# Optimization experiments

Measured on AMD Instinct MI355X. Metric: run time of the kernel, lower is better.

## Reference

```python
import jax, jax.numpy as jnp
import numpy as np
import math

B, L, HID = 2, 2048, 1024
NH, DH = 16, 64
MASK_VAL = -1000000000.0  # half_precision_flag == False


def setup_inputs() -> dict:
    key = jax.random.key(0)
    ks = jax.random.split(key, 12)
    s = 0.02
    return {
        "queries": jax.random.normal(ks[0], (B, L, HID), jnp.float32),
        "keys": jax.random.normal(ks[1], (B, L, HID), jnp.float32),
        "values": jax.random.normal(ks[2], (B, L, HID), jnp.float32),
        "mask": jax.random.randint(ks[3], (B, L, L), 0, 2, jnp.int32),
        "Wq": jax.random.normal(ks[4], (HID, NH * DH), jnp.float32) * s,
        "bq": jnp.zeros((NH * DH,), jnp.float32),
        "Wk": jax.random.normal(ks[5], (HID, NH * DH), jnp.float32) * s,
        "bk": jnp.zeros((NH * DH,), jnp.float32),
        "Wv": jax.random.normal(ks[6], (HID, NH * DH), jnp.float32) * s,
        "bv": jnp.zeros((NH * DH,), jnp.float32),
        "Wo": jax.random.normal(ks[7], (NH * DH, HID), jnp.float32) * s,
        "bo": jnp.zeros((HID,), jnp.float32),
    }


def reference(queries, keys, values, mask, Wq, bq, Wk, bk, Wv, bv, Wo, bo):
    # Linear projections: (B, L, NH*DH)
    q = queries @ Wq + bq
    k = keys @ Wk + bk
    v = values @ Wv + bv
    # FAITHFUL to original: raw .view(B, NH, -1, DH) without transpose
    q = q.reshape(B, NH, L, DH)
    k = k.reshape(B, NH, L, DH)
    v = v.reshape(B, NH, L, DH)
    # scaled dot-product scores: (B, NH, L, L)
    scores = jnp.einsum("bhqd,bhkd->bhqk", q, k) / math.sqrt(DH)
    scores = jnp.where(mask[:, None, :, :] == 0, MASK_VAL, scores)
    probs = jax.nn.softmax(scores, axis=-1)  # dropout p=0 -> identity
    ctx = jnp.einsum("bhqk,bhkd->bhqd", probs, v)  # (B, NH, L, DH)
    # transpose(1,2) then flatten heads, as in original
    ctx = ctx.transpose(0, 2, 1, 3).reshape(B, L, NH * DH)
    return ctx @ Wo + bo
```

## Files before the change

kernel.cpp:

```cpp
#include <hip/hip_runtime.h>
#include <stdint.h>

typedef __bf16 bf16;
typedef __bf16 bf16x8 __attribute__((ext_vector_type(8)));
typedef __bf16 bf16x4 __attribute__((ext_vector_type(4)));
typedef float  f32x4  __attribute__((ext_vector_type(4)));
typedef short  s16x4  __attribute__((ext_vector_type(4)));
typedef unsigned long long ull;

#define GLOAD16(gptr, lptr)                                                     \
  __builtin_amdgcn_global_load_lds(                                             \
      (const __attribute__((address_space(1))) void*)(gptr),                    \
      (__attribute__((address_space(3))) void*)(lptr), 16, 0, 0)

#define MFMA16(a, b, c) __builtin_amdgcn_mfma_f32_16x16x32_bf16((a), (b), (c), 0, 0, 0)
#define MFMA16K16(a, b, c) __builtin_amdgcn_mfma_f32_16x16x16bf16_1k((a), (b), (c), 0, 0, 0)

static constexpr int B_ = 2, L_ = 2048, NH_ = 16, DH_ = 64;
static constexpr float QSCALE = 0.18033688011112042f;

__global__ __launch_bounds__(256) void k_prep(const float* __restrict__ q,
                                              const float* __restrict__ k,
                                              const float* __restrict__ v,
                                              const int* __restrict__ mask,
                                              const float* __restrict__ wq,
                                              const float* __restrict__ wk,
                                              const float* __restrict__ wv,
                                              const float* __restrict__ wo,
                                              bf16* __restrict__ X,
                                              bf16* __restrict__ Wt,
                                              ull* __restrict__ mb) {
  __shared__ float t[32][33];
  const int bid = blockIdx.x, tid = threadIdx.x;
  if (bid < 32768) {
    int tt = bid * 256 + tid;
    ull bal = __ballot(mask[tt] != 0);
    if ((tid & 63) == 0) mb[tt >> 6] = bal;
  } else if (bid < 45056) {
    int u = bid - 32768;
    int z = u >> 12, x = u & 4095;
    const float* in = z == 0 ? q : (z == 1 ? k : v);
    bf16* out = X + (size_t)z * 4194304;
    int i = x * 256 + tid;
    const float4 f = ((const float4*)in)[i];
    bf16x4 o = {(bf16)f.x, (bf16)f.y, (bf16)f.z, (bf16)f.w};
    ((bf16x4*)out)[i] = o;
  } else {
    int u = bid - 45056;
    int z = u >> 10, rem = u & 1023;
    const float* in = z == 0 ? wq : (z == 1 ? wk : (z == 2 ? wv : wo));
    bf16* out = Wt + (size_t)z * 1048576;
    int bx = (rem & 31) * 32, by = (rem >> 5) * 32;
    int x = tid & 31, y = tid >> 5;
#pragma unroll
    for (int r = 0; r < 4; ++r)
      t[y + r * 8][x] = in[(size_t)(by + y + r * 8) * 1024 + bx + x];
    __syncthreads();
#pragma unroll
    for (int r = 0; r < 4; ++r)
      out[(size_t)(bx + y + r * 8) * 1024 + by + x] = (bf16)t[x][y + r * 8];
  }
}

__global__ __launch_bounds__(256) void k_gemm3(const bf16* __restrict__ Xb,
                                               const bf16* __restrict__ Wb,
                                               const float* __restrict__ b0,
                                               const float* __restrict__ b1,
                                               const float* __restrict__ b2,
                                               bf16* __restrict__ Ob) {
  const int z = blockIdx.z;
  const bf16* A  = Xb + (size_t)z * 4194304;
  const bf16* Bt = Wb + (size_t)z * 1048576;
  const float* bias = z == 0 ? b0 : (z == 1 ? b1 : b2);
  bf16* C = Ob + (size_t)z * 4194304;
  const int m0 = blockIdx.y * 128, n0 = blockIdx.x * 128;
  __shared__ __align__(16) bf16 As[128 * 32];
  __shared__ __align__(16) bf16 Bs[128 * 32];
  const int tid = threadIdx.x, lane = tid & 63, w = tid >> 6, quad = lane >> 4, l15 = lane & 15;
  const int wm = (w & 1) * 64, wn = (w >> 1) * 64;
  f32x4 acc[4][4] = {};
  for (int kt = 0; kt < 32; ++kt) {
    const int kk = kt * 32;
#pragma unroll
    for (int i = 0; i < 2; ++i) {
      int s = tid + i * 256;
      int r = s >> 2, c = (s & 3) ^ ((r >> 1) & 3);
      GLOAD16(A + (size_t)(m0 + r) * 1024 + kk + c * 8, As + s * 8);
      GLOAD16(Bt + (size_t)(n0 + r) * 1024 + kk + c * 8, Bs + s * 8);
    }
    __syncthreads();
    bf16x8 af[4], bb[4];
#pragma unroll
    for (int i = 0; i < 4; ++i) {
      int ra = wm + i * 16 + l15, rb = wn + i * 16 + l15;
      af[i] = *(const bf16x8*)(As + (ra * 4 + (quad ^ ((ra >> 1) & 3))) * 8);
      bb[i] = *(const bf16x8*)(Bs + (rb * 4 + (quad ^ ((rb >> 1) & 3))) * 8);
    }
#pragma unroll
    for (int mi = 0; mi < 4; ++mi)
#pragma unroll
      for (int ni = 0; ni < 4; ++ni)
        acc[mi][ni] = MFMA16(af[mi], bb[ni], acc[mi][ni]);
    __syncthreads();
  }
  const float scale = (z == 0) ? QSCALE : 1.0f;
#pragma unroll
  for (int mi = 0; mi < 4; ++mi)
#pragma unroll
    for (int ni = 0; ni < 4; ++ni) {
      int row = m0 + wm + mi * 16 + quad * 4;
      int col = n0 + wn + ni * 16 + l15;
      float bz = bias[col];
      if (z == 2) {
        int b_ = row >> 11, l = row & 2047;
        int hh = l >> 7;
        int i0 = (l & 127) * 16 + (col >> 6);
        int d  = col & 63;
        bf16* dst = C + (size_t)(b_ * 16 + hh) * 131072;
#pragma unroll
        for (int r = 0; r < 4; ++r) {
          int iK = i0 + 16 * r;
          dst[((size_t)(iK >> 2) * 64 + d) * 4 + (iK & 3)] = (bf16)(acc[mi][ni][r] + bz);
        }
      } else {
#pragma unroll
        for (int r = 0; r < 4; ++r)
          C[(size_t)(row + r) * 1024 + col] = (bf16)((acc[mi][ni][r] + bz) * scale);
      }
    }
}

__global__ __launch_bounds__(256) void k_gemmo(const bf16* __restrict__ A,
                                               const bf16* __restrict__ Bt,
                                               const float* __restrict__ bias,
                                               float* __restrict__ C) {
  const int m0 = blockIdx.y * 64, n0 = blockIdx.x * 128;
  __shared__ __align__(16) bf16 As[64 * 32];
  __shared__ __align__(16) bf16 Bs[128 * 32];
  const int tid = threadIdx.x, lane = tid & 63, w = tid >> 6, quad = lane >> 4, l15 = lane & 15;
  const int wn = w * 32;
  f32x4 acc[4][2] = {};
  for (int kt = 0; kt < 32; ++kt) {
    const int kk = kt * 32;
    {
      int r = tid >> 2, c = (tid & 3) ^ ((r >> 1) & 3);
      GLOAD16(A + (size_t)(m0 + r) * 1024 + kk + c * 8, As + tid * 8);
    }
#pragma unroll
    for (int i = 0; i < 2; ++i) {
      int s = tid + i * 256;
      int r = s >> 2, c = (s & 3) ^ ((r >> 1) & 3);
      GLOAD16(Bt + (size_t)(n0 + r) * 1024 + kk + c * 8, Bs + s * 8);
    }
    __syncthreads();
    bf16x8 af[4], bb[2];
#pragma unroll
    for (int i = 0; i < 4; ++i) {
      int ra = i * 16 + l15;
      af[i] = *(const bf16x8*)(As + (ra * 4 + (quad ^ ((ra >> 1) & 3))) * 8);
    }
#pragma unroll
    for (int i = 0; i < 2; ++i) {
      int rb = wn + i * 16 + l15;
      bb[i] = *(const bf16x8*)(Bs + (rb * 4 + (quad ^ ((rb >> 1) & 3))) * 8);
    }
#pragma unroll
    for (int mi = 0; mi < 4; ++mi)
#pragma unroll
      for (int ni = 0; ni < 2; ++ni)
        acc[mi][ni] = MFMA16(af[mi], bb[ni], acc[mi][ni]);
    __syncthreads();
  }
#pragma unroll
  for (int mi = 0; mi < 4; ++mi)
#pragma unroll
    for (int ni = 0; ni < 2; ++ni) {
      int row = m0 + mi * 16 + quad * 4;
      int col = n0 + wn + ni * 16 + l15;
      float bz = bias[col];
#pragma unroll
      for (int r = 0; r < 4; ++r)
        C[(size_t)(row + r) * 1024 + col] = acc[mi][ni][r] + bz;
    }
}

__global__ __launch_bounds__(512) void k_flash(const bf16* __restrict__ Qp,
                                               const bf16* __restrict__ Kp,
                                               const bf16* __restrict__ Vtp,
                                               const ull* __restrict__ mb,
                                               bf16* __restrict__ ctx) {
  const int b = blockIdx.z, h = blockIdx.y, q0 = blockIdx.x * 128;
  const size_t HEAD = 131072;
  const bf16* Q  = Qp  + ((size_t)b * NH_ + h) * HEAD;
  const bf16* K  = Kp  + ((size_t)b * NH_ + h) * HEAD;
  const bf16* Vt = Vtp + ((size_t)b * NH_ + h) * HEAD;
  const ull* mrow = mb + (size_t)b * L_ * 32;

  __shared__ __align__(16) bf16 Ks[2][64 * 64];
  __shared__ __align__(16) bf16 Vs[2][64 * 64];
  __shared__ __align__(16) ull  Ms[2][256];

  const int tid = threadIdx.x, lane = tid & 63, w = tid >> 6, quad = lane >> 4, l15 = lane & 15;

  bf16x8 qf[2];
#pragma unroll
  for (int ks = 0; ks < 2; ++ks)
    qf[ks] = *(const bf16x8*)(Q + (size_t)(q0 + w * 16 + l15) * 64 + ks * 32 + quad * 8);

  {
    int s = tid;
    int key = s >> 3, c = (s & 7) ^ (key & 7);
    GLOAD16(K + (size_t)key * 64 + c * 8, Ks[0] + s * 8);
    GLOAD16(Vt + (size_t)s * 8, Vs[0] + s * 8);
  }
  if (w < 2) {
    int r = w * 64 + lane;
    GLOAD16(mrow + (size_t)(q0 + r) * 32, (bf16*)&Ms[0][0] + r * 8);
  }
  __syncthreads();

  f32x4 accO[4] = {};
  f32x4 accL = {};
  const s16x4 onesf = {0x3F80, 0x3F80, 0x3F80, 0x3F80};

  for (int kt = 0; kt < 32; ++kt) {
    const int cur = kt & 1;
    if (kt + 1 < 32) {
      const int nxt = cur ^ 1;
      int s = tid;
      int key = s >> 3, c = (s & 7) ^ (key & 7);
      GLOAD16(K + (size_t)((kt + 1) * 64 + key) * 64 + c * 8, Ks[nxt] + s * 8);
      GLOAD16(Vt + (size_t)(kt + 1) * 4096 + s * 8, Vs[nxt] + s * 8);
      if ((kt & 1) && w < 2) {
        int r = w * 64 + lane;
        GLOAD16(mrow + (size_t)(q0 + r) * 32 + (kt + 1),
                (bf16*)&Ms[((kt + 1) >> 1) & 1][0] + r * 8);
      }
    }

    f32x4 st[4] = {};
#pragma unroll
    for (int ks = 0; ks < 2; ++ks)
#pragma unroll
      for (int kb = 0; kb < 4; ++kb) {
        int key = kb * 16 + l15;
        bf16x8 kf = *(const bf16x8*)(Ks[cur] + (key * 8 + ((ks * 4 + quad) ^ (key & 7))) * 8);
        st[kb] = MFMA16(kf, qf[ks], st[kb]);
      }

    const ull* Mcur = Ms[(kt >> 1) & 1];
    const ull word = Mcur[(w * 16 + l15) * 2 + cur];
    s16x4 pf[4];
#pragma unroll
    for (int kb = 0; kb < 4; ++kb) {
      const unsigned nib = (unsigned)(word >> (kb * 16 + quad * 4)) & 0xFu;
      float p0 = (nib & 1u) ? __builtin_amdgcn_exp2f(st[kb][0]) : 0.f;
      float p1 = (nib & 2u) ? __builtin_amdgcn_exp2f(st[kb][1]) : 0.f;
      float p2 = (nib & 4u) ? __builtin_amdgcn_exp2f(st[kb][2]) : 0.f;
      float p3 = (nib & 8u) ? __builtin_amdgcn_exp2f(st[kb][3]) : 0.f;
      bf16x4 pb = {(bf16)p0, (bf16)p1, (bf16)p2, (bf16)p3};
      pf[kb] = __builtin_bit_cast(s16x4, pb);
    }

#pragma unroll
    for (int kb = 0; kb < 4; ++kb)
      accL = MFMA16K16(pf[kb], onesf, accL);

#pragma unroll
    for (int kb = 0; kb < 4; ++kb)
#pragma unroll
      for (int db = 0; db < 4; ++db) {
        s16x4 vf = *(const s16x4*)(Vs[cur] + ((size_t)((kb * 4 + quad) * 64 + db * 16 + l15)) * 4);
        accO[db] = MFMA16K16(pf[kb], vf, accO[db]);
      }
    __syncthreads();
  }

  float rl[4];
#pragma unroll
  for (int r = 0; r < 4; ++r) rl[r] = 1.0f / accL[r];
#pragma unroll
  for (int db = 0; db < 4; ++db) {
    const int col = h * 64 + db * 16 + l15;
#pragma unroll
    for (int r = 0; r < 4; ++r) {
      const int rowg = q0 + w * 16 + quad * 4 + r;
      ctx[((size_t)b * L_ + rowg) * 1024 + col] = (bf16)(accO[db][r] * rl[r]);
    }
  }
}

extern "C" void kernel_launch(void* const* d_in, const int* in_sizes, int n_in,
                              void* d_out, int out_size, void* d_ws, size_t ws_size,
                              hipStream_t stream) {
  (void)in_sizes; (void)n_in; (void)out_size; (void)ws_size;
  const float* q    = (const float*)d_in[0];
  const float* k    = (const float*)d_in[1];
  const float* v    = (const float*)d_in[2];
  const int*   mask = (const int*)d_in[3];
  const float* Wq = (const float*)d_in[4];
  const float* bq = (const float*)d_in[5];
  const float* Wk = (const float*)d_in[6];
  const float* bk = (const float*)d_in[7];
  const float* Wv = (const float*)d_in[8];
  const float* bv = (const float*)d_in[9];
  const float* Wo = (const float*)d_in[10];
  const float* bo = (const float*)d_in[11];
  float* out = (float*)d_out;

  char* ws = (char*)d_ws;
  const size_t SX = (size_t)4096 * 1024 * 2;
  const size_t SW = (size_t)1024 * 1024 * 2;
  bf16* X   = (bf16*)(ws);
  bf16* Wt  = (bf16*)(ws + 3 * SX);
  bf16* QKV = (bf16*)(ws + 3 * SX + 4 * SW);
  bf16* Qp  = QKV;
  bf16* Kp  = QKV + 4194304;
  bf16* Vtp = QKV + 2 * 4194304;
  bf16* Ctx = (bf16*)(ws + 6 * SX + 4 * SW);
  ull* mbits = (ull*)(ws + 7 * SX + 4 * SW);

  dim3 blk(256);
  k_prep<<<49152, blk, 0, stream>>>(q, k, v, mask, Wq, Wk, Wv, Wo, X, Wt, mbits);

  k_gemm3<<<dim3(8, 32, 3), blk, 0, stream>>>(X, Wt, bq, bk, bv, QKV);

  k_flash<<<dim3(16, NH_, B_), dim3(512), 0, stream>>>(Qp, Kp, Vtp, mbits, Ctx);

  k_gemmo<<<dim3(8, 64), blk, 0, stream>>>(Ctx, Wt + 3 * 1048576, bo, out);
}
```

Baseline: 268.2 us.

## Use 32x32 MFMA tiles in flash attention with key-split waves and LDS reduction

Rewrites the attention inner loop to use 32x32x16 bf16 MFMA instead of 16x16 tiles. Each pair of waves now shares a 32-query block and splits the 64 keys of each tile in half; the partial outputs and row sums are combined through shared memory at the end. Probabilities are repacked into MFMA A-operand layout with permlane32_swap, and launch bounds are raised to request higher occupancy. This is meant to cut MFMA issue count and per-wave LDS fragment traffic, at the cost of an extra reduction pass, cross-lane shuffles and added register pressure.

```diff
diff --git a/kernel.cpp b/kernel.cpp
--- a/kernel.cpp
+++ b/kernel.cpp
@@ -4,8 +4,13 @@
 typedef __bf16 bf16;
 typedef __bf16 bf16x8 __attribute__((ext_vector_type(8)));
 typedef __bf16 bf16x4 __attribute__((ext_vector_type(4)));
+typedef __bf16 bf16x2 __attribute__((ext_vector_type(2)));
 typedef float  f32x4  __attribute__((ext_vector_type(4)));
+typedef float  f32x16 __attribute__((ext_vector_type(16)));
 typedef short  s16x4  __attribute__((ext_vector_type(4)));
+typedef short  s16x8  __attribute__((ext_vector_type(8)));
+typedef unsigned int u32x2 __attribute__((ext_vector_type(2)));
+typedef unsigned int u32x4 __attribute__((ext_vector_type(4)));
 typedef unsigned long long ull;
 
 #define GLOAD16(gptr, lptr)                                                     \
@@ -14,7 +19,7 @@
       (__attribute__((address_space(3))) void*)(lptr), 16, 0, 0)
 
 #define MFMA16(a, b, c) __builtin_amdgcn_mfma_f32_16x16x32_bf16((a), (b), (c), 0, 0, 0)
-#define MFMA16K16(a, b, c) __builtin_amdgcn_mfma_f32_16x16x16bf16_1k((a), (b), (c), 0, 0, 0)
+#define MFMA32(a, b, c) __builtin_amdgcn_mfma_f32_32x32x16_bf16((a), (b), (c), 0, 0, 0)
 
 static constexpr int B_ = 2, L_ = 2048, NH_ = 16, DH_ = 64;
 static constexpr float QSCALE = 0.18033688011112042f;
@@ -184,11 +189,16 @@
     }
 }
 
-__global__ __launch_bounds__(512) void k_flash(const bf16* __restrict__ Qp,
-                                               const bf16* __restrict__ Kp,
-                                               const bf16* __restrict__ Vtp,
-                                               const ull* __restrict__ mb,
-                                               bf16* __restrict__ ctx) {
+static __device__ __forceinline__ unsigned pack2(float a, float b) {
+  bf16x2 t = {(bf16)a, (bf16)b};
+  return __builtin_bit_cast(unsigned, t);
+}
+
+__global__ __launch_bounds__(512, 4) void k_flash(const bf16* __restrict__ Qp,
+                                                  const bf16* __restrict__ Kp,
+                                                  const bf16* __restrict__ Vtp,
+                                                  const ull* __restrict__ mb,
+                                                  bf16* __restrict__ ctx) {
   const int b = blockIdx.z, h = blockIdx.y, q0 = blockIdx.x * 128;
   const size_t HEAD = 131072;
   const bf16* Q  = Qp  + ((size_t)b * NH_ + h) * HEAD;
@@ -196,96 +206,124 @@
   const bf16* Vt = Vtp + ((size_t)b * NH_ + h) * HEAD;
   const ull* mrow = mb + (size_t)b * L_ * 32;
 
-  __shared__ __align__(16) bf16 Ks[2][64 * 64];
-  __shared__ __align__(16) bf16 Vs[2][64 * 64];
-  __shared__ __align__(16) ull  Ms[2][256];
-
-  const int tid = threadIdx.x, lane = tid & 63, w = tid >> 6, quad = lane >> 4, l15 = lane & 15;
-
-  bf16x8 qf[2];
-#pragma unroll
-  for (int ks = 0; ks < 2; ++ks)
-    qf[ks] = *(const bf16x8*)(Q + (size_t)(q0 + w * 16 + l15) * 64 + ks * 32 + quad * 8);
+  __shared__ __align__(16) unsigned char RAW[36864];
+  bf16* Ksb = (bf16*)RAW;
+  bf16* Vsb = (bf16*)(RAW + 16384);
+  ull*  Msb = (ull*)(RAW + 32768);
+
+  const int tid = threadIdx.x, lane = tid & 63, w = tid >> 6;
+  const int hi = lane >> 5, l31 = lane & 31;
+  const int kh = w & 1, qq = w >> 1;
+
+  bf16x8 qf[4];
+#pragma unroll
+  for (int ks = 0; ks < 4; ++ks)
+    qf[ks] = *(const bf16x8*)(Q + (size_t)(q0 + qq * 32 + l31) * 64 + ks * 16 + hi * 8);
 
   {
     int s = tid;
     int key = s >> 3, c = (s & 7) ^ (key & 7);
-    GLOAD16(K + (size_t)key * 64 + c * 8, Ks[0] + s * 8);
-    GLOAD16(Vt + (size_t)s * 8, Vs[0] + s * 8);
+    GLOAD16(K + (size_t)key * 64 + c * 8, Ksb + s * 8);
+    GLOAD16(Vt + (size_t)s * 8, Vsb + s * 8);
   }
   if (w < 2) {
     int r = w * 64 + lane;
-    GLOAD16(mrow + (size_t)(q0 + r) * 32, (bf16*)&Ms[0][0] + r * 8);
+    GLOAD16(mrow + (size_t)(q0 + r) * 32, (bf16*)Msb + r * 8);
   }
   __syncthreads();
 
-  f32x4 accO[4] = {};
-  f32x4 accL = {};
-  const s16x4 onesf = {0x3F80, 0x3F80, 0x3F80, 0x3F80};
+  f32x16 accO0 = {}, accO1 = {}, accL = {};
+  const s16x8 one8s = {0x3F80, 0x3F80, 0x3F80, 0x3F80, 0x3F80, 0x3F80, 0x3F80, 0x3F80};
+  const bf16x8 ones8 = __builtin_bit_cast(bf16x8, one8s);
 
   for (int kt = 0; kt < 32; ++kt) {
     const int cur = kt & 1;
+    const bf16* Kc = Ksb + cur * 4096;
+    const bf16* Vc = Vsb + cur * 4096;
     if (kt + 1 < 32) {
       const int nxt = cur ^ 1;
       int s = tid;
       int key = s >> 3, c = (s & 7) ^ (key & 7);
-      GLOAD16(K + (size_t)((kt + 1) * 64 + key) * 64 + c * 8, Ks[nxt] + s * 8);
-      GLOAD16(Vt + (size_t)(kt + 1) * 4096 + s * 8, Vs[nxt] + s * 8);
+      GLOAD16(K + (size_t)((kt + 1) * 64 + key) * 64 + c * 8, Ksb + nxt * 4096 + s * 8);
+      GLOAD16(Vt + (size_t)(kt + 1) * 4096 + s * 8, Vsb + nxt * 4096 + s * 8);
       if ((kt & 1) && w < 2) {
         int r = w * 64 + lane;
         GLOAD16(mrow + (size_t)(q0 + r) * 32 + (kt + 1),
-                (bf16*)&Ms[((kt + 1) >> 1) & 1][0] + r * 8);
+                (bf16*)Msb + (((kt + 1) >> 1) & 1) * 1024 + r * 8);
       }
     }
 
-    f32x4 st[4] = {};
-#pragma unroll
-    for (int ks = 0; ks < 2; ++ks)
-#pragma unroll
-      for (int kb = 0; kb < 4; ++kb) {
-        int key = kb * 16 + l15;
-        bf16x8 kf = *(const bf16x8*)(Ks[cur] + (key * 8 + ((ks * 4 + quad) ^ (key & 7))) * 8);
-        st[kb] = MFMA16(kf, qf[ks], st[kb]);
-      }
-
-    const ull* Mcur = Ms[(kt >> 1) & 1];
-    const ull word = Mcur[(w * 16 + l15) * 2 + cur];
-    s16x4 pf[4];
-#pragma unroll
-    for (int kb = 0; kb < 4; ++kb) {
-      const unsigned nib = (unsigned)(word >> (kb * 16 + quad * 4)) & 0xFu;
-      float p0 = (nib & 1u) ? __builtin_amdgcn_exp2f(st[kb][0]) : 0.f;
-      float p1 = (nib & 2u) ? __builtin_amdgcn_exp2f(st[kb][1]) : 0.f;
-      float p2 = (nib & 4u) ? __builtin_amdgcn_exp2f(st[kb][2]) : 0.f;
-      float p3 = (nib & 8u) ? __builtin_amdgcn_exp2f(st[kb][3]) : 0.f;
-      bf16x4 pb = {(bf16)p0, (bf16)p1, (bf16)p2, (bf16)p3};
-      pf[kb] = __builtin_bit_cast(s16x4, pb);
-    }
-
-#pragma unroll
-    for (int kb = 0; kb < 4; ++kb)
-      accL = MFMA16K16(pf[kb], onesf, accL);
-
-#pragma unroll
-    for (int kb = 0; kb < 4; ++kb)
-#pragma unroll
-      for (int db = 0; db < 4; ++db) {
-        s16x4 vf = *(const s16x4*)(Vs[cur] + ((size_t)((kb * 4 + quad) * 64 + db * 16 + l15)) * 4);
-        accO[db] = MFMA16K16(pf[kb], vf, accO[db]);
-      }
-    __syncthreads();
-  }
-
-  float rl[4];
-#pragma unroll
-  for (int r = 0; r < 4; ++r) rl[r] = 1.0f / accL[r];
-#pragma unroll
-  for (int db = 0; db < 4; ++db) {
-    const int col = h * 64 + db * 16 + l15;
-#pragma unroll
-    for (int r = 0; r < 4; ++r) {
-      const int rowg = q0 + w * 16 + quad * 4 + r;
-      ctx[((size_t)b * L_ + rowg) * 1024 + col] = (bf16)(accO[db][r] * rl[r]);
+    f32x16 st = {};
+    const int key = kh * 32 + l31;
+#pragma unroll
+    for (int ks = 0; ks < 4; ++ks) {
+      bf16x8 kf = *(const bf16x8*)(Kc + (key * 8 + ((ks * 2 + hi) ^ (key & 7))) * 8);
+      st = MFMA32(kf, qf[ks], st);
+    }
+
+    const ull word = Msb[((kt >> 1) & 1) * 256 + (qq * 32 + l31) * 2 + cur];
+    const unsigned w32 = (unsigned)(word >> (kh * 32 + 4 * hi));
+#pragma unroll
+    for (int r = 0; r < 16; ++r) {
+      const int bit = (r >> 2) * 8 + (r & 3);
+      st[r] = (w32 >> bit) & 1u ? __builtin_amdgcn_exp2f(st[r]) : 0.f;
+    }
+
+    bf16x8 af[2];
+#pragma unroll
+    for (int ks2 = 0; ks2 < 2; ++ks2) {
+      const int bb = ks2 * 8;
+      unsigned c0 = pack2(st[bb + 0], st[bb + 1]);
+      unsigned c1 = pack2(st[bb + 2], st[bb + 3]);
+      unsigned c2 = pack2(st[bb + 4], st[bb + 5]);
+      unsigned c3 = pack2(st[bb + 6], st[bb + 7]);
+      u32x2 s0 = __builtin_amdgcn_permlane32_swap(c0, c2, false, false);
+      u32x2 s1 = __builtin_amdgcn_permlane32_swap(c1, c3, false, false);
+      u32x4 a4 = {s0.x, s1.x, s0.y, s1.y};
+      af[ks2] = __builtin_bit_cast(bf16x8, a4);
+    }
+
+    accL = MFMA32(af[0], ones8, accL);
+    accL = MFMA32(af[1], ones8, accL);
+
+#pragma unroll
+    for (int ks2 = 0; ks2 < 2; ++ks2) {
+      const int vb = ((kh * 32 + ks2 * 16 + hi * 8) >> 2) * 64 + l31;
+      s16x4 a0 = *(const s16x4*)(Vc + (size_t)vb * 4);
+      s16x4 a1 = *(const s16x4*)(Vc + (size_t)(vb + 64) * 4);
+      s16x4 b0 = *(const s16x4*)(Vc + (size_t)(vb + 32) * 4);
+      s16x4 b1 = *(const s16x4*)(Vc + (size_t)(vb + 96) * 4);
+      bf16x8 v0 = __builtin_bit_cast(bf16x8, __builtin_shufflevector(a0, a1, 0, 1, 2, 3, 4, 5, 6, 7));
+      bf16x8 v1 = __builtin_bit_cast(bf16x8, __builtin_shufflevector(b0, b1, 0, 1, 2, 3, 4, 5, 6, 7));
+      accO0 = MFMA32(af[ks2], v0, accO0);
+      accO1 = MFMA32(af[ks2], v1, accO1);
+    }
+    __syncthreads();
+  }
+
+  float* red  = (float*)RAW;
+  float* redL = (float*)(RAW + 32768);
+  if (kh == 1) {
+#pragma unroll
+    for (int r = 0; r < 16; ++r) {
+      const int qrel = (r & 3) + 8 * (r >> 2) + 4 * hi;
+      red[qq * 2048 + qrel * 64 + l31]      = accO0[r];
+      red[qq * 2048 + qrel * 64 + 32 + l31] = accO1[r];
+      if (l31 == 0) redL[qq * 32 + qrel] = accL[r];
+    }
+  }
+  __syncthreads();
+  if (kh == 0) {
+#pragma unroll
+    for (int r = 0; r < 16; ++r) {
+      const int qrel = (r & 3) + 8 * (r >> 2) + 4 * hi;
+      const float ls = accL[r] + redL[qq * 32 + qrel];
+      const float rl = 1.0f / ls;
+      const float o0 = accO0[r] + red[qq * 2048 + qrel * 64 + l31];
+      const float o1 = accO1[r] + red[qq * 2048 + qrel * 64 + 32 + l31];
+      const int rowg = q0 + qq * 32 + qrel;
+      ctx[((size_t)b * L_ + rowg) * 1024 + h * 64 + l31]      = (bf16)(o0 * rl);
+      ctx[((size_t)b * L_ + rowg) * 1024 + h * 64 + 32 + l31] = (bf16)(o1 * rl);
     }
   }
 }
```

After: 267.8 us. Within noise of the previous version (-0.2%).
